# Optimization experiments

Measured on AMD Instinct MI355X. Metric: run time of the kernel, lower is better.

The kernel has to match this reference:

```python
import jax, jax.numpy as jnp
import numpy as np

NUM_HEADS = 12
NUM_LANDMARKS = 64
EPS_REG = 1e-4


def setup_inputs() -> dict:
    key = jax.random.key(0)
    k1, k2, k3 = jax.random.split(key, 3)
    B, N, C = 4, 4096, 768
    x = jax.random.normal(k1, (B, N, C), dtype=jnp.float32)
    w_qkv = jax.random.normal(k2, (3 * C, C), dtype=jnp.float32) * (C ** -0.5)
    w_proj = jax.random.normal(k3, (C, C), dtype=jnp.float32) * (C ** -0.5)
    b_proj = jnp.zeros((C,), dtype=jnp.float32)
    return {"x": x, "w_qkv": w_qkv, "w_proj": w_proj, "b_proj": b_proj}


def _landmark_pool(t, m):
    # t: [B, H, N, D]; assumes N % m == 0 (true for chosen shapes)
    B, H, N, D = t.shape
    seg = N // m
    return t.reshape(B, H, m, seg, D).mean(axis=3)


def reference(x, w_qkv, w_proj, b_proj):
    B, N, C = x.shape
    H = NUM_HEADS
    D = C // H
    m = min(NUM_LANDMARKS, N)
    scale = D ** -0.5

    qkv = x @ w_qkv.T                              # [B, N, 3C]
    qkv = qkv.reshape(B, N, 3, H, D).transpose(2, 0, 3, 1, 4)
    q, k, v = qkv[0], qkv[1], qkv[2]               # [B, H, N, D]

    q_lm = _landmark_pool(q, m)                    # [B, H, m, D]
    k_lm = _landmark_pool(k, m)                    # [B, H, m, D]

    attn_q_km = jax.nn.softmax(jnp.einsum('bhnd,bhmd->bhnm', q, k_lm) * scale, axis=-1)
    attn_qm_km = jax.nn.softmax(jnp.einsum('bhld,bhmd->bhlm', q_lm, k_lm) * scale, axis=-1)
    attn_qm_k = jax.nn.softmax(jnp.einsum('bhmd,bhnd->bhmn', q_lm, k) * scale, axis=-1)

    eye = jnp.eye(m, dtype=attn_qm_km.dtype)
    inv_mid = jnp.linalg.inv(attn_qm_km + EPS_REG * eye)   # [B, H, m, m]

    out = attn_q_km @ (inv_mid @ (attn_qm_k @ v))          # [B, H, N, D]
    out = out.transpose(0, 2, 1, 3).reshape(B, N, C)
    out = out @ w_proj.T + b_proj
    return out
```

## Files before the change

### kernel.cpp

```cpp
#include <hip/hip_runtime.h>

typedef unsigned short u16;
typedef __attribute__((ext_vector_type(8))) short bf16x8;
typedef __attribute__((ext_vector_type(8))) unsigned short u16x8;
typedef __attribute__((ext_vector_type(4))) unsigned short u16x4;
typedef __attribute__((ext_vector_type(4))) float f32x4;

#define NB 4
#define NH 12
#define NSEQ 4096
#define NC 768
#define ND 64
#define NM 64
#define NBH 48

__device__ __forceinline__ float b2f(u16 u){ unsigned v = ((unsigned)u)<<16; return __builtin_bit_cast(float, v); }
__device__ __forceinline__ u16 f2b(float f){ unsigned u = __builtin_bit_cast(unsigned, f); u = u + 0x7FFFu + ((u>>16)&1u); return (u16)(u>>16); }
__device__ __forceinline__ void split2(float f, u16& h, u16& l){
  h = f2b(f);
  l = f2b(f - b2f(h));
}

typedef const __attribute__((address_space(1))) unsigned int guint;
typedef __attribute__((address_space(3))) unsigned int luint;
__device__ __forceinline__ void gload16(const void* g, void* l){
  __builtin_amdgcn_global_load_lds((guint*)g, (luint*)l, 16, 0, 0);
}

__device__ __forceinline__ f32x4 mfma16x16(bf16x8 a, bf16x8 b, f32x4 c){
  return __builtin_amdgcn_mfma_f32_16x16x32_bf16(a, b, c, 0, 0, 0);
}

__global__ __launch_bounds__(256) void k_split(const float* __restrict__ src, u16* __restrict__ dh,
                                               u16* __restrict__ dl, int n4){
  int i = blockIdx.x*256 + threadIdx.x;
  if (i >= n4) return;
  f32x4 v = ((const f32x4*)src)[i];
  u16x4 hh, ll;
  #pragma unroll
  for (int e=0;e<4;++e){ u16 hb, lb; split2(v[e], hb, lb); hh[e]=hb; ll[e]=lb; }
  ((u16x4*)dh)[i] = hh; ((u16x4*)dl)[i] = ll;
}

__global__ __launch_bounds__(256) void k_qkv(const u16* __restrict__ xh, const u16* __restrict__ xl,
                                             const u16* __restrict__ wh, const u16* __restrict__ wl,
                                             u16* __restrict__ qh, u16* __restrict__ ql,
                                             u16* __restrict__ kh, u16* __restrict__ kl,
                                             u16* __restrict__ vh, u16* __restrict__ vl){
  __shared__ u16 Ah[8192], Al[8192], Bh[8192], Bl[8192];
  const int K = NC;
  int tid = threadIdx.x, wave = tid>>6, lane = tid&63;
  int wm = wave>>1, wn = wave&1;
  int m0 = blockIdx.y*128, n0 = blockIdx.x*128;
  int srow = lane>>3, scol = (lane&7)*8;
  const u16* src0; u16* dst0;
  if (wave==0){ src0 = xh + (size_t)m0*K; dst0 = Ah; }
  else if (wave==1){ src0 = xl + (size_t)m0*K; dst0 = Al; }
  else if (wave==2){ src0 = wh + (size_t)n0*K; dst0 = Bh; }
  else            { src0 = wl + (size_t)n0*K; dst0 = Bl; }
  f32x4 acc[4][4] = {};
  for (int k0=0; k0<K; k0+=64){
    #pragma unroll
    for (int it=0; it<16; ++it){
      int r = it*8;
      gload16(&src0[(size_t)(r+srow)*K + k0 + scol], &dst0[r*64]);
    }
    __syncthreads();
    #pragma unroll
    for (int kk=0; kk<2; ++kk){
      int koff = kk*32 + (lane>>4)*8;
      bf16x8 a_h[4], a_l[4], b_h[4], b_l[4];
      #pragma unroll
      for (int i=0;i<4;++i){
        int ro = (wm*64+i*16+(lane&15))*64 + koff;
        a_h[i] = *(const bf16x8*)&Ah[ro]; a_l[i] = *(const bf16x8*)&Al[ro];
      }
      #pragma unroll
      for (int j=0;j<4;++j){
        int ro = (wn*64+j*16+(lane&15))*64 + koff;
        b_h[j] = *(const bf16x8*)&Bh[ro]; b_l[j] = *(const bf16x8*)&Bl[ro];
      }
      #pragma unroll
      for (int i=0;i<4;++i)
        #pragma unroll
        for (int j=0;j<4;++j){
          acc[i][j] = mfma16x16(a_h[i], b_h[j], acc[i][j]);
          acc[i][j] = mfma16x16(a_h[i], b_l[j], acc[i][j]);
          acc[i][j] = mfma16x16(a_l[i], b_h[j], acc[i][j]);
        }
    }
    __syncthreads();
  }
  int rb = (lane>>4)*4, cb = lane&15;
  #pragma unroll
  for (int j=0;j<4;++j){
    int gn = n0 + wn*64 + j*16 + cb;
    int s = gn/768; int rem = gn - s*768; int hd = rem>>6, d = rem&63;
    u16* dh = (s==0)? qh : (s==1)? kh : vh;
    u16* dl = (s==0)? ql : (s==1)? kl : vl;
    #pragma unroll
    for (int i=0;i<4;++i){
      #pragma unroll
      for (int r=0;r<4;++r){
        int gm = m0 + wm*64 + i*16 + rb + r;
        int b_ = gm>>12, n = gm & 4095;
        size_t idx = (((size_t)(b_*NH + hd))*NSEQ + n)*ND + d;
        u16 hb, lb; split2(acc[i][j][r], hb, lb);
        dh[idx] = hb; dl[idx] = lb;
      }
    }
  }
}

__global__ __launch_bounds__(256) void k_proj(const u16* __restrict__ Hh, const u16* __restrict__ Hl,
                                              const u16* __restrict__ wh, const u16* __restrict__ wl,
                                              const float* __restrict__ bias, float* __restrict__ out){
  __shared__ u16 Ah[8192], Al[8192], Bh[8192], Bl[8192];
  const int K = NC;
  int tid = threadIdx.x, wave = tid>>6, lane = tid&63;
  int wm = wave>>1, wn = wave&1;
  int m0 = blockIdx.y*128, n0 = blockIdx.x*128;
  int srow = lane>>3, scol = (lane&7)*8;
  const u16* src0; u16* dst0;
  if (wave==0){ src0 = Hh + (size_t)m0*K; dst0 = Ah; }
  else if (wave==1){ src0 = Hl + (size_t)m0*K; dst0 = Al; }
  else if (wave==2){ src0 = wh + (size_t)n0*K; dst0 = Bh; }
  else            { src0 = wl + (size_t)n0*K; dst0 = Bl; }
  f32x4 acc[4][4] = {};
  for (int k0=0; k0<K; k0+=64){
    #pragma unroll
    for (int it=0; it<16; ++it){
      int r = it*8;
      gload16(&src0[(size_t)(r+srow)*K + k0 + scol], &dst0[r*64]);
    }
    __syncthreads();
    #pragma unroll
    for (int kk=0; kk<2; ++kk){
      int koff = kk*32 + (lane>>4)*8;
      bf16x8 a_h[4], a_l[4], b_h[4], b_l[4];
      #pragma unroll
      for (int i=0;i<4;++i){
        int ro = (wm*64+i*16+(lane&15))*64 + koff;
        a_h[i] = *(const bf16x8*)&Ah[ro]; a_l[i] = *(const bf16x8*)&Al[ro];
      }
      #pragma unroll
      for (int j=0;j<4;++j){
        int ro = (wn*64+j*16+(lane&15))*64 + koff;
        b_h[j] = *(const bf16x8*)&Bh[ro]; b_l[j] = *(const bf16x8*)&Bl[ro];
      }
      #pragma unroll
      for (int i=0;i<4;++i)
        #pragma unroll
        for (int j=0;j<4;++j){
          acc[i][j] = mfma16x16(a_h[i], b_h[j], acc[i][j]);
          acc[i][j] = mfma16x16(a_h[i], b_l[j], acc[i][j]);
          acc[i][j] = mfma16x16(a_l[i], b_h[j], acc[i][j]);
        }
    }
    __syncthreads();
  }
  int rb = (lane>>4)*4, cb = lane&15;
  #pragma unroll
  for (int j=0;j<4;++j){
    int gn = n0 + wn*64 + j*16 + cb;
    float bb = bias[gn];
    #pragma unroll
    for (int i=0;i<4;++i){
      #pragma unroll
      for (int r=0;r<4;++r){
        int gm = m0 + wm*64 + i*16 + rb + r;
        out[(size_t)gm*NC + gn] = acc[i][j][r] + bb;
      }
    }
  }
}

__global__ __launch_bounds__(64) void k_pool(const u16* __restrict__ qh, const u16* __restrict__ ql,
                                             const u16* __restrict__ kh, const u16* __restrict__ kl,
                                             float* __restrict__ qlmf, float* __restrict__ klmf,
                                             u16* __restrict__ qlmh, u16* __restrict__ qlml,
                                             u16* __restrict__ klmh, u16* __restrict__ klml){
  int l = blockIdx.x, bh = blockIdx.y, d = threadIdx.x;
  size_t base = ((size_t)bh*NSEQ + l*64)*ND + d;
  float sq = 0.f, sk = 0.f;
  #pragma unroll 8
  for (int j=0;j<64;++j){
    size_t o = base + (size_t)j*ND;
    sq += b2f(qh[o]) + b2f(ql[o]);
    sk += b2f(kh[o]) + b2f(kl[o]);
  }
  sq *= (1.f/64.f); sk *= (1.f/64.f);
  size_t o = ((size_t)bh*NM + l)*ND + d;
  qlmf[o] = sq; klmf[o] = sk;
  u16 hb, lb;
  split2(sq, hb, lb); qlmh[o] = hb; qlml[o] = lb;
  split2(sk, hb, lb); klmh[o] = hb; klml[o] = lb;
}

__global__ __launch_bounds__(256) void k_s2(const u16* __restrict__ qlmh, const u16* __restrict__ qlml,
                                            const u16* __restrict__ kh, const u16* __restrict__ kl,
                                            float* __restrict__ s2f){
  int chunk = blockIdx.x, bh = blockIdx.y;
  int tid = threadIdx.x, wave = tid>>6, lane = tid&63;
  const u16* Ahp = qlmh + (size_t)bh*NM*ND;
  const u16* Alp = qlml + (size_t)bh*NM*ND;
  const u16* Bhp = kh + (size_t)bh*NSEQ*ND;
  const u16* Blp = kl + (size_t)bh*NSEQ*ND;
  int nbase = chunk*256 + wave*64;
  f32x4 acc[4][4] = {};
  #pragma unroll
  for (int kk=0; kk<2; ++kk){
    int koff = kk*32 + (lane>>4)*8;
    bf16x8 a_h[4], a_l[4], b_h[4], b_l[4];
    #pragma unroll
    for (int i=0;i<4;++i){
      size_t ro = (size_t)(i*16+(lane&15))*ND + koff;
      a_h[i] = *(const bf16x8*)&Ahp[ro]; a_l[i] = *(const bf16x8*)&Alp[ro];
    }
    #pragma unroll
    for (int j=0;j<4;++j){
      size_t ro = (size_t)(nbase + j*16 + (lane&15))*ND + koff;
      b_h[j] = *(const bf16x8*)&Bhp[ro]; b_l[j] = *(const bf16x8*)&Blp[ro];
    }
    #pragma unroll
    for (int i=0;i<4;++i)
      #pragma unroll
      for (int j=0;j<4;++j){
        acc[i][j] = mfma16x16(a_h[i], b_h[j], acc[i][j]);
        acc[i][j] = mfma16x16(a_h[i], b_l[j], acc[i][j]);
        acc[i][j] = mfma16x16(a_l[i], b_h[j], acc[i][j]);
      }
  }
  int rb = (lane>>4)*4, cb = lane&15;
  #pragma unroll
  for (int i=0;i<4;++i)
    #pragma unroll
    for (int j=0;j<4;++j)
      #pragma unroll
      for (int r=0;r<4;++r){
        int l = i*16 + rb + r; int n = nbase + j*16 + cb;
        s2f[((size_t)bh*NM + l)*NSEQ + n] = acc[i][j][r]*0.125f;
      }
}

__global__ __launch_bounds__(256) void k_sm(float* __restrict__ s2region){
  int row = blockIdx.x;
  int tid = threadIdx.x, lane = tid&63, wid = tid>>6;
  __shared__ float redm[4], reds[4];
  const float* src = s2region + (size_t)row*NSEQ;
  const f32x4* ps = (const f32x4*)(src + (size_t)tid*16);
  f32x4 v0 = ps[0], v1 = ps[1], v2 = ps[2], v3 = ps[3];
  float vals[16];
  #pragma unroll
  for (int e=0;e<4;++e){ vals[e]=v0[e]; vals[4+e]=v1[e]; vals[8+e]=v2[e]; vals[12+e]=v3[e]; }
  float mx = -1e30f;
  #pragma unroll
  for (int j=0;j<16;++j) mx = fmaxf(mx, vals[j]);
  for (int off=32; off; off>>=1) mx = fmaxf(mx, __shfl_xor(mx, off));
  if (lane==0) redm[wid] = mx;
  __syncthreads();
  mx = fmaxf(fmaxf(redm[0],redm[1]), fmaxf(redm[2],redm[3]));
  float s = 0.f;
  #pragma unroll
  for (int j=0;j<16;++j){ vals[j] = __expf(vals[j]-mx); s += vals[j]; }
  for (int off=32; off; off>>=1) s += __shfl_xor(s, off);
  if (lane==0) reds[wid] = s;
  __syncthreads();
  s = reds[0]+reds[1]+reds[2]+reds[3];
  float inv = 1.f/s;
  u16* rh = (u16*)s2region + (size_t)row*8192;
  u16* rl = rh + 4096;
  u16x8 oh0, oh1, ol0, ol1;
  #pragma unroll
  for (int j=0;j<8;++j){
    u16 hb, lb;
    split2(vals[j]*inv, hb, lb);   oh0[j]=hb; ol0[j]=lb;
    split2(vals[8+j]*inv, hb, lb); oh1[j]=hb; ol1[j]=lb;
  }
  ((u16x8*)(rh + (size_t)tid*16))[0] = oh0;
  ((u16x8*)(rh + (size_t)tid*16))[1] = oh1;
  ((u16x8*)(rl + (size_t)tid*16))[0] = ol0;
  ((u16x8*)(rl + (size_t)tid*16))[1] = ol1;
}

__global__ __launch_bounds__(256) void k_transpose(const u16* __restrict__ vh, const u16* __restrict__ vl,
                                                   u16* __restrict__ vTh, u16* __restrict__ vTl){
  __shared__ u16 th[64*65], tl_[64*65];
  int bh = blockIdx.y, n0 = blockIdx.x*64, tid = threadIdx.x;
  #pragma unroll
  for (int jj=0;jj<16;++jj){
    int idx = tid + jj*256; int n = idx>>6, d = idx&63;
    size_t g = ((size_t)bh*NSEQ + n0 + n)*ND + d;
    th[n*65+d] = vh[g]; tl_[n*65+d] = vl[g];
  }
  __syncthreads();
  #pragma unroll
  for (int jj=0;jj<16;++jj){
    int idx = tid + jj*256; int d = idx>>6, n = idx&63;
    size_t g = ((size_t)bh*ND + d)*NSEQ + n0 + n;
    vTh[g] = th[n*65+d]; vTl[g] = tl_[n*65+d];
  }
}

__global__ __launch_bounds__(256) void k_t1(const u16* __restrict__ p2base, const u16* __restrict__ vTh,
                                            const u16* __restrict__ vTl, float* __restrict__ t1p){
  int kb = blockIdx.x, bh = blockIdx.y;
  int tid = threadIdx.x, wave = tid>>6, lane = tid&63;
  int arow = wave*16 + (lane&15);
  const u16* rowp = p2base + (size_t)(bh*64 + arow)*8192;
  const u16* Bh = vTh + (size_t)bh*ND*NSEQ;
  const u16* Bl = vTl + (size_t)bh*ND*NSEQ;
  f32x4 acc[4] = {};
  for (int ks=0; ks<16; ++ks){
    int koff = kb*512 + ks*32 + (lane>>4)*8;
    bf16x8 a_h = *(const bf16x8*)&rowp[koff];
    bf16x8 a_l = *(const bf16x8*)&rowp[4096 + koff];
    #pragma unroll
    for (int j=0;j<4;++j){
      size_t ro = (size_t)(j*16+(lane&15))*NSEQ + koff;
      bf16x8 b_h = *(const bf16x8*)&Bh[ro];
      bf16x8 b_l = *(const bf16x8*)&Bl[ro];
      acc[j] = mfma16x16(a_h, b_h, acc[j]);
      acc[j] = mfma16x16(a_h, b_l, acc[j]);
      acc[j] = mfma16x16(a_l, b_h, acc[j]);
    }
  }
  int rb = (lane>>4)*4, cb = lane&15;
  #pragma unroll
  for (int j=0;j<4;++j)
    #pragma unroll
    for (int r=0;r<4;++r){
      int l = wave*16 + rb + r; int d = j*16 + cb;
      t1p[((size_t)(kb*NBH + bh)*NM + l)*ND + d] = acc[j][r];
    }
}

__global__ __launch_bounds__(256) void k_mid(const float* __restrict__ qlmf, const float* __restrict__ klmf,
                                            const float* __restrict__ t1p,
                                            u16* __restrict__ w2th, u16* __restrict__ w2tl){
  __shared__ float M[64*68];
  __shared__ float T[64*68];
  __shared__ int piv_s;
  int bh = blockIdx.x, tid = threadIdx.x;
  int r = tid>>2, qd = tid&3;
  const float* qrow  = qlmf + (size_t)bh*NM*ND + r*64;
  const float* kbase = klmf + (size_t)bh*NM*ND;
  float qv[64];
  #pragma unroll
  for (int e=0;e<16;++e){
    f32x4 t4 = ((const f32x4*)qrow)[e];
    qv[e*4]=t4[0]; qv[e*4+1]=t4[1]; qv[e*4+2]=t4[2]; qv[e*4+3]=t4[3];
  }
  float sv[16];
  #pragma unroll
  for (int mi=0;mi<16;++mi){
    const float* krow = kbase + (size_t)(qd*16+mi)*64;
    float a = 0.f;
    #pragma unroll
    for (int e=0;e<16;++e){
      f32x4 k4 = ((const f32x4*)krow)[e];
      a += qv[e*4]*k4[0] + qv[e*4+1]*k4[1] + qv[e*4+2]*k4[2] + qv[e*4+3]*k4[3];
    }
    sv[mi] = a*0.125f;
  }
  float mx = sv[0];
  #pragma unroll
  for (int mi=1;mi<16;++mi) mx = fmaxf(mx, sv[mi]);
  mx = fmaxf(mx, __shfl_xor(mx,1)); mx = fmaxf(mx, __shfl_xor(mx,2));
  float sum = 0.f;
  #pragma unroll
  for (int mi=0;mi<16;++mi){ sv[mi] = __expf(sv[mi]-mx); sum += sv[mi]; }
  sum += __shfl_xor(sum,1); sum += __shfl_xor(sum,2);
  float sinv = 1.f/sum;
  #pragma unroll
  for (int mi=0;mi<16;++mi){
    int m = qd*16+mi;
    float p = sv[mi]*sinv;
    if (m == r) p += 1e-4f;
    M[r*68+m] = p;
  }
  #pragma unroll
  for (int q=0;q<4;++q){
    int c = qd*16 + q*4;
    f32x4 a = {};
    #pragma unroll
    for (int kb=0;kb<8;++kb)
      a += *(const f32x4*)&t1p[((size_t)(kb*NBH + bh)*NM + r)*ND + c];
    *(f32x4*)&T[r*68+c] = a;
  }
  __syncthreads();
  for (int kp=0; kp<64; ++kp){
    if (tid < 64){
      float val = (tid >= kp) ? fabsf(M[tid*68+kp]) : -1.f;
      int idx = tid;
      #pragma unroll
      for (int off=32; off; off>>=1){
        float ov = __shfl_xor(val, off); int oi = __shfl_xor(idx, off);
        if (ov > val || (ov == val && oi < idx)){ val = ov; idx = oi; }
      }
      if (tid == 0) piv_s = idx;
    }
    __syncthreads();
    int p = piv_s;
    if (r == kp){
      float pinv = 1.f / M[p*68+kp];
      f32x4 mk[4], mp[4], tk[4], tp_[4];
      #pragma unroll
      for (int q=0;q<4;++q){
        int c = qd*16 + q*4;
        mk[q] = *(const f32x4*)&M[kp*68+c]; mp[q] = *(const f32x4*)&M[p*68+c];
        tk[q] = *(const f32x4*)&T[kp*68+c]; tp_[q] = *(const f32x4*)&T[p*68+c];
      }
      #pragma unroll
      for (int q=0;q<4;++q){
        int c = qd*16 + q*4;
        *(f32x4*)&M[p*68+c] = mk[q];       *(f32x4*)&T[p*68+c] = tk[q];
        *(f32x4*)&M[kp*68+c] = mp[q]*pinv; *(f32x4*)&T[kp*68+c] = tp_[q]*pinv;
      }
    }
    __syncthreads();
    if (r != kp){
      float f = M[r*68+kp];
      #pragma unroll
      for (int q=0;q<4;++q){
        int c = qd*16 + q*4;
        f32x4 pm = *(const f32x4*)&M[kp*68+c];
        f32x4 om = *(const f32x4*)&M[r*68+c];
        *(f32x4*)&M[r*68+c] = om - f*pm;
        f32x4 pt = *(const f32x4*)&T[kp*68+c];
        f32x4 ot = *(const f32x4*)&T[r*68+c];
        *(f32x4*)&T[r*68+c] = ot - f*pt;
      }
    }
    __syncthreads();
  }
  int d = tid>>2, qs = tid&3;
  #pragma unroll
  for (int li=0; li<16; ++li){
    int l = qs*16 + li;
    float xv = T[l*68 + d];
    u16 hb, lb; split2(xv, hb, lb);
    size_t o = ((size_t)bh*ND + d)*NM + l;
    w2th[o] = hb; w2tl[o] = lb;
  }
}

__global__ __launch_bounds__(256) void k_final(const u16* __restrict__ qh, const u16* __restrict__ ql,
                                               const u16* __restrict__ klmh, const u16* __restrict__ klml,
                                               const u16* __restrict__ w2th, const u16* __restrict__ w2tl,
                                               u16* __restrict__ Hh, u16* __restrict__ Hl){
  __shared__ u16 Ph[4*4096], Pl[4*4096];
  int chunk = blockIdx.x, bh = blockIdx.y;
  int b_ = bh/NH, hd = bh - b_*NH;
  int tid = threadIdx.x, wave = tid>>6, lane = tid&63;
  int n0 = chunk*256 + wave*64;
  const u16* qhp = qh + ((size_t)bh*NSEQ + n0)*ND;
  const u16* qlp = ql + ((size_t)bh*NSEQ + n0)*ND;
  const u16* Kh = klmh + (size_t)bh*NM*ND;
  const u16* Kl = klml + (size_t)bh*NM*ND;
  const u16* Wh = w2th + (size_t)bh*ND*NM;
  const u16* Wl = w2tl + (size_t)bh*ND*NM;
  u16* Phw = Ph + wave*4096;
  u16* Plw = Pl + wave*4096;
  f32x4 accs[4][4] = {};
  #pragma unroll
  for (int kk=0; kk<2; ++kk){
    int koff = kk*32 + (lane>>4)*8;
    bf16x8 a_h[4], a_l[4], b_h[4], b_l[4];
    #pragma unroll
    for (int i=0;i<4;++i){
      size_t ro = (size_t)(i*16+(lane&15))*ND + koff;
      a_h[i] = *(const bf16x8*)&qhp[ro]; a_l[i] = *(const bf16x8*)&qlp[ro];
    }
    #pragma unroll
    for (int j=0;j<4;++j){
      size_t ro = (size_t)(j*16+(lane&15))*ND + koff;
      b_h[j] = *(const bf16x8*)&Kh[ro]; b_l[j] = *(const bf16x8*)&Kl[ro];
    }
    #pragma unroll
    for (int i=0;i<4;++i)
      #pragma unroll
      for (int j=0;j<4;++j){
        accs[i][j] = mfma16x16(a_h[i], b_h[j], accs[i][j]);
        accs[i][j] = mfma16x16(a_h[i], b_l[j], accs[i][j]);
        accs[i][j] = mfma16x16(a_l[i], b_h[j], accs[i][j]);
      }
  }
  #pragma unroll
  for (int i=0;i<4;++i)
    #pragma unroll
    for (int j=0;j<4;++j) accs[i][j] *= 0.125f;
  int rb = (lane>>4)*4, cb = lane&15;
  #pragma unroll
  for (int i=0;i<4;++i){
    #pragma unroll
    for (int r=0;r<4;++r){
      float mx = -1e30f;
      #pragma unroll
      for (int j=0;j<4;++j) mx = fmaxf(mx, accs[i][j][r]);
      #pragma unroll
      for (int off=1; off<16; off<<=1) mx = fmaxf(mx, __shfl_xor(mx, off));
      float e[4]; float sum = 0.f;
      #pragma unroll
      for (int j=0;j<4;++j){ e[j] = __expf(accs[i][j][r]-mx); sum += e[j]; }
      #pragma unroll
      for (int off=1; off<16; off<<=1) sum += __shfl_xor(sum, off);
      float inv = 1.f/sum;
      int row = i*16 + rb + r;
      #pragma unroll
      for (int j=0;j<4;++j){
        u16 hb, lb; split2(e[j]*inv, hb, lb);
        Phw[row*64 + j*16 + cb] = hb;
        Plw[row*64 + j*16 + cb] = lb;
      }
    }
  }
  __syncthreads();
  f32x4 acco[4][4] = {};
  #pragma unroll
  for (int kk=0; kk<2; ++kk){
    int koff = kk*32 + (lane>>4)*8;
    bf16x8 a_h[4], a_l[4], b_h[4], b_l[4];
    #pragma unroll
    for (int i=0;i<4;++i){
      int ro = (i*16+(lane&15))*64 + koff;
      a_h[i] = *(const bf16x8*)&Phw[ro]; a_l[i] = *(const bf16x8*)&Plw[ro];
    }
    #pragma unroll
    for (int j=0;j<4;++j){
      size_t ro = (size_t)(j*16+(lane&15))*64 + koff;
      b_h[j] = *(const bf16x8*)&Wh[ro]; b_l[j] = *(const bf16x8*)&Wl[ro];
    }
    #pragma unroll
    for (int i=0;i<4;++i)
      #pragma unroll
      for (int j=0;j<4;++j){
        acco[i][j] = mfma16x16(a_h[i], b_h[j], acco[i][j]);
        acco[i][j] = mfma16x16(a_h[i], b_l[j], acco[i][j]);
        acco[i][j] = mfma16x16(a_l[i], b_h[j], acco[i][j]);
      }
  }
  #pragma unroll
  for (int i=0;i<4;++i)
    #pragma unroll
    for (int j=0;j<4;++j)
      #pragma unroll
      for (int r=0;r<4;++r){
        int n = n0 + i*16 + rb + r;
        int d = j*16 + cb;
        size_t o = ((size_t)(b_*NSEQ + n))*NC + hd*64 + d;
        u16 hb, lb; split2(acco[i][j][r], hb, lb);
        Hh[o] = hb; Hl[o] = lb;
      }
}

__global__ void k_sent(float* out){ out[0] = 1.0e9f; }

#define OFF_QH     0ull
#define OFF_QL     25165824ull
#define OFF_KH     50331648ull
#define OFF_KL     75497472ull
#define OFF_VH     100663296ull
#define OFF_VL     125829120ull
#define OFF_S2     150994944ull
#define OFF_QLMF   201326592ull
#define OFF_KLMF   202113024ull
#define OFF_QLMH   202899456ull
#define OFF_QLML   203292672ull
#define OFF_KLMH   203685888ull
#define OFF_KLML   204079104ull
#define OFF_W2TH   204472320ull
#define OFF_W2TL   204865536ull
#define OFF_T1P    205258752ull
#define OFF_WQH    211550208ull
#define OFF_WQL    215089152ull
#define OFF_WPH    218628096ull
#define OFF_WPL    219807744ull
#define WS_NEEDED  220987392ull

extern "C" void kernel_launch(void* const* d_in, const int* in_sizes, int n_in,
                              void* d_out, int out_size, void* d_ws, size_t ws_size,
                              hipStream_t stream){
  const float* x     = (const float*)d_in[0];
  const float* wqkv  = (const float*)d_in[1];
  const float* wproj = (const float*)d_in[2];
  const float* bproj = (const float*)d_in[3];
  float* out = (float*)d_out;
  char* ws = (char*)d_ws;
  if (ws_size < WS_NEEDED){ k_sent<<<1,1,0,stream>>>(out); return; }
  u16* qh = (u16*)(ws + OFF_QH);  u16* ql = (u16*)(ws + OFF_QL);
  u16* kh = (u16*)(ws + OFF_KH);  u16* kl = (u16*)(ws + OFF_KL);
  u16* vh = (u16*)(ws + OFF_VH);  u16* vl = (u16*)(ws + OFF_VL);
  u16* vTh = kh; u16* vTl = kl;
  u16* xh = (u16*)(ws + OFF_S2);
  u16* xl = (u16*)(ws + OFF_S2 + 25165824ull);
  float* s2f = (float*)(ws + OFF_S2);
  u16* p2base = (u16*)(ws + OFF_S2);
  u16* Hh = (u16*)(ws + OFF_S2);
  u16* Hl = (u16*)(ws + OFF_S2 + 25165824ull);
  float* qlmf = (float*)(ws + OFF_QLMF);
  float* klmf = (float*)(ws + OFF_KLMF);
  u16* qlmh = (u16*)(ws + OFF_QLMH); u16* qlml = (u16*)(ws + OFF_QLML);
  u16* klmh = (u16*)(ws + OFF_KLMH); u16* klml = (u16*)(ws + OFF_KLML);
  u16* w2th = (u16*)(ws + OFF_W2TH); u16* w2tl = (u16*)(ws + OFF_W2TL);
  float* t1p = (float*)(ws + OFF_T1P);
  u16* wqh = (u16*)(ws + OFF_WQH); u16* wql = (u16*)(ws + OFF_WQL);
  u16* wph = (u16*)(ws + OFF_WPH); u16* wpl = (u16*)(ws + OFF_WPL);

  k_split    <<<12288, 256, 0, stream>>>(x, xh, xl, 3145728);
  k_split    <<<1728,  256, 0, stream>>>(wqkv, wqh, wql, 442368);
  k_split    <<<576,   256, 0, stream>>>(wproj, wph, wpl, 147456);
  k_qkv      <<<dim3(18,128), 256, 0, stream>>>(xh, xl, wqh, wql, qh, ql, kh, kl, vh, vl);
  k_pool     <<<dim3(64,48),   64, 0, stream>>>(qh, ql, kh, kl, qlmf, klmf, qlmh, qlml, klmh, klml);
  k_s2       <<<dim3(16,48),  256, 0, stream>>>(qlmh, qlml, kh, kl, s2f);
  k_sm       <<<3072,         256, 0, stream>>>(s2f);
  k_transpose<<<dim3(64,48),  256, 0, stream>>>(vh, vl, vTh, vTl);
  k_t1       <<<dim3(8,48),   256, 0, stream>>>(p2base, vTh, vTl, t1p);
  k_mid      <<<48,           256, 0, stream>>>(qlmf, klmf, t1p, w2th, w2tl);
  k_final    <<<dim3(16,48),  256, 0, stream>>>(qh, ql, klmh, klml, w2th, w2tl, Hh, Hl);
  k_proj     <<<dim3(6,128),  256, 0, stream>>>(Hh, Hl, wph, wpl, bproj, out);
}
```

Baseline: 559.0 us.

## Replace QKV and projection GEMMs with double-buffered 256x256 tile kernel

Both split-bf16 GEMMs now run through one templated 512-thread kernel with 256x256 tiles. It double-buffers LDS using async global-to-LDS loads, applies an XOR swizzle against bank conflicts, remaps blocks for L2 locality, and raises wave priority around the MFMA clusters. The QKV epilogue writes V directly in transposed layout, which removes the separate transpose kernel. The larger tiles mean fewer blocks (576 and 192), which risks poor CU utilisation on the projection GEMM. The 128 KB LDS footprint also limits occupancy.

```diff
diff --git a/kernel.cpp b/kernel.cpp
--- a/kernel.cpp
+++ b/kernel.cpp
@@ -42,134 +42,124 @@
   ((u16x4*)dh)[i] = hh; ((u16x4*)dl)[i] = ll;
 }
 
-__global__ __launch_bounds__(256) void k_qkv(const u16* __restrict__ xh, const u16* __restrict__ xl,
-                                             const u16* __restrict__ wh, const u16* __restrict__ wl,
-                                             u16* __restrict__ qh, u16* __restrict__ ql,
-                                             u16* __restrict__ kh, u16* __restrict__ kl,
-                                             u16* __restrict__ vh, u16* __restrict__ vl){
-  __shared__ u16 Ah[8192], Al[8192], Bh[8192], Bl[8192];
+template<int MODE>
+__global__ __launch_bounds__(512,2) void k_gemm256(
+    const u16* __restrict__ Agh, const u16* __restrict__ Agl,
+    const u16* __restrict__ Bgh, const u16* __restrict__ Bgl,
+    u16* __restrict__ q_h, u16* __restrict__ q_l,
+    u16* __restrict__ k_h, u16* __restrict__ k_l,
+    u16* __restrict__ v_h, u16* __restrict__ v_l,
+    const float* __restrict__ bias, float* __restrict__ outf,
+    int nbx){
+  __shared__ u16 lds[65536];
   const int K = NC;
   int tid = threadIdx.x, wave = tid>>6, lane = tid&63;
-  int wm = wave>>1, wn = wave&1;
-  int m0 = blockIdx.y*128, n0 = blockIdx.x*128;
-  int srow = lane>>3, scol = (lane&7)*8;
-  const u16* src0; u16* dst0;
-  if (wave==0){ src0 = xh + (size_t)m0*K; dst0 = Ah; }
-  else if (wave==1){ src0 = xl + (size_t)m0*K; dst0 = Al; }
-  else if (wave==2){ src0 = wh + (size_t)n0*K; dst0 = Bh; }
-  else            { src0 = wl + (size_t)n0*K; dst0 = Bl; }
-  f32x4 acc[4][4] = {};
-  for (int k0=0; k0<K; k0+=64){
-    #pragma unroll
-    for (int it=0; it<16; ++it){
-      int r = it*8;
-      gload16(&src0[(size_t)(r+srow)*K + k0 + scol], &dst0[r*64]);
-    }
-    __syncthreads();
-    #pragma unroll
-    for (int kk=0; kk<2; ++kk){
-      int koff = kk*32 + (lane>>4)*8;
-      bf16x8 a_h[4], a_l[4], b_h[4], b_l[4];
-      #pragma unroll
-      for (int i=0;i<4;++i){
-        int ro = (wm*64+i*16+(lane&15))*64 + koff;
-        a_h[i] = *(const bf16x8*)&Ah[ro]; a_l[i] = *(const bf16x8*)&Al[ro];
-      }
+  int wm = wave>>2, wn = wave&3;
+  int nwg = gridDim.x, bid = blockIdx.x;
+  int swz = (bid&7)*(nwg>>3) + (bid>>3);
+  int by = swz / nbx, bx = swz - by*nbx;
+  int m0 = by*256, n0 = bx*256;
+  const u16* sbase[8]; int soff[8];
+  #pragma unroll
+  for (int s=0;s<8;++s){
+    int c = s*512 + tid;
+    int mat = c>>10, idx = c&1023, row = idx>>2, slot = idx&3;
+    int gslot = slot ^ ((row>>1)&3);
+    const u16* g;
+    if (mat==0)      g = Agh + (size_t)(m0+row)*K + gslot*8;
+    else if (mat==1) g = Agl + (size_t)(m0+row)*K + gslot*8;
+    else if (mat==2) g = Bgh + (size_t)(n0+row)*K + gslot*8;
+    else             g = Bgl + (size_t)(n0+row)*K + gslot*8;
+    sbase[s] = g;
+    soff[s] = mat*8192 + row*32 + slot*8;
+  }
+  int fr = ((lane&15)>>1)&3;
+  int sl = ((lane>>4) ^ fr)*8;
+  int aoff = (wm*128 + (lane&15))*32 + sl;
+  int boff = (wn*64  + (lane&15))*32 + sl;
+  #pragma unroll
+  for (int s=0;s<8;++s) gload16(sbase[s], &lds[soff[s]]);
+  asm volatile("s_waitcnt vmcnt(0)" ::: "memory");
+  __builtin_amdgcn_s_barrier();
+  __builtin_amdgcn_sched_barrier(0);
+  f32x4 acc[8][4] = {};
+  for (int t=0; t<24; ++t){
+    int cur = (t&1)*32768, nxt = ((t+1)&1)*32768;
+    int k0 = (t+1)*32;
+    bool st = (t < 23);
+    const u16* Ab = &lds[cur];
+    const u16* Bb = &lds[cur + 16384];
+    if (st){
+      gload16(sbase[0]+k0, &lds[nxt+soff[0]]); gload16(sbase[1]+k0, &lds[nxt+soff[1]]);
+      gload16(sbase[2]+k0, &lds[nxt+soff[2]]); gload16(sbase[3]+k0, &lds[nxt+soff[3]]);
+    }
+    bf16x8 bh[4], bl[4];
+    #pragma unroll
+    for (int j=0;j<4;++j){
+      bh[j] = *(const bf16x8*)&Bb[boff + j*512];
+      bl[j] = *(const bf16x8*)&Bb[8192 + boff + j*512];
+    }
+    #pragma unroll
+    for (int p=0;p<4;++p){
+      if (st && p==1){
+        gload16(sbase[4]+k0, &lds[nxt+soff[4]]); gload16(sbase[5]+k0, &lds[nxt+soff[5]]);
+        gload16(sbase[6]+k0, &lds[nxt+soff[6]]); gload16(sbase[7]+k0, &lds[nxt+soff[7]]);
+      }
+      bf16x8 ah0 = *(const bf16x8*)&Ab[aoff + (2*p)*512];
+      bf16x8 al0 = *(const bf16x8*)&Ab[8192 + aoff + (2*p)*512];
+      bf16x8 ah1 = *(const bf16x8*)&Ab[aoff + (2*p+1)*512];
+      bf16x8 al1 = *(const bf16x8*)&Ab[8192 + aoff + (2*p+1)*512];
+      __builtin_amdgcn_s_setprio(1);
       #pragma unroll
       for (int j=0;j<4;++j){
-        int ro = (wn*64+j*16+(lane&15))*64 + koff;
-        b_h[j] = *(const bf16x8*)&Bh[ro]; b_l[j] = *(const bf16x8*)&Bl[ro];
-      }
-      #pragma unroll
-      for (int i=0;i<4;++i)
+        acc[2*p][j]   = mfma16x16(ah0, bh[j], acc[2*p][j]);
+        acc[2*p][j]   = mfma16x16(ah0, bl[j], acc[2*p][j]);
+        acc[2*p][j]   = mfma16x16(al0, bh[j], acc[2*p][j]);
+        acc[2*p+1][j] = mfma16x16(ah1, bh[j], acc[2*p+1][j]);
+        acc[2*p+1][j] = mfma16x16(ah1, bl[j], acc[2*p+1][j]);
+        acc[2*p+1][j] = mfma16x16(al1, bh[j], acc[2*p+1][j]);
+      }
+      __builtin_amdgcn_s_setprio(0);
+      if (p < 3) __builtin_amdgcn_s_barrier();
+    }
+    asm volatile("s_waitcnt vmcnt(0)" ::: "memory");
+    __builtin_amdgcn_s_barrier();
+    __builtin_amdgcn_sched_barrier(0);
+  }
+  int rb = (lane>>4)*4, cb = lane&15;
+  if (MODE == 0){
+    #pragma unroll
+    for (int j=0;j<4;++j){
+      int gn = n0 + wn*64 + j*16 + cb;
+      int s = gn/768; int rem = gn - s*768; int hd = rem>>6, d = rem&63;
+      u16* dh = (s==0)? q_h : (s==1)? k_h : v_h;
+      u16* dl = (s==0)? q_l : (s==1)? k_l : v_l;
+      #pragma unroll
+      for (int i=0;i<8;++i){
         #pragma unroll
-        for (int j=0;j<4;++j){
-          acc[i][j] = mfma16x16(a_h[i], b_h[j], acc[i][j]);
-          acc[i][j] = mfma16x16(a_h[i], b_l[j], acc[i][j]);
-          acc[i][j] = mfma16x16(a_l[i], b_h[j], acc[i][j]);
+        for (int r=0;r<4;++r){
+          int gm = m0 + wm*128 + i*16 + rb + r;
+          int b_ = gm>>12, n = gm & 4095;
+          size_t idx;
+          if (s==2) idx = (((size_t)(b_*NH + hd))*ND + d)*NSEQ + n;
+          else      idx = (((size_t)(b_*NH + hd))*NSEQ + n)*ND + d;
+          u16 hb2, lb2; split2(acc[i][j][r], hb2, lb2);
+          dh[idx] = hb2; dl[idx] = lb2;
         }
-    }
-    __syncthreads();
-  }
-  int rb = (lane>>4)*4, cb = lane&15;
-  #pragma unroll
-  for (int j=0;j<4;++j){
-    int gn = n0 + wn*64 + j*16 + cb;
-    int s = gn/768; int rem = gn - s*768; int hd = rem>>6, d = rem&63;
-    u16* dh = (s==0)? qh : (s==1)? kh : vh;
-    u16* dl = (s==0)? ql : (s==1)? kl : vl;
-    #pragma unroll
-    for (int i=0;i<4;++i){
-      #pragma unroll
-      for (int r=0;r<4;++r){
-        int gm = m0 + wm*64 + i*16 + rb + r;
-        int b_ = gm>>12, n = gm & 4095;
-        size_t idx = (((size_t)(b_*NH + hd))*NSEQ + n)*ND + d;
-        u16 hb, lb; split2(acc[i][j][r], hb, lb);
-        dh[idx] = hb; dl[idx] = lb;
-      }
-    }
-  }
-}
-
-__global__ __launch_bounds__(256) void k_proj(const u16* __restrict__ Hh, const u16* __restrict__ Hl,
-                                              const u16* __restrict__ wh, const u16* __restrict__ wl,
-                                              const float* __restrict__ bias, float* __restrict__ out){
-  __shared__ u16 Ah[8192], Al[8192], Bh[8192], Bl[8192];
-  const int K = NC;
-  int tid = threadIdx.x, wave = tid>>6, lane = tid&63;
-  int wm = wave>>1, wn = wave&1;
-  int m0 = blockIdx.y*128, n0 = blockIdx.x*128;
-  int srow = lane>>3, scol = (lane&7)*8;
-  const u16* src0; u16* dst0;
-  if (wave==0){ src0 = Hh + (size_t)m0*K; dst0 = Ah; }
-  else if (wave==1){ src0 = Hl + (size_t)m0*K; dst0 = Al; }
-  else if (wave==2){ src0 = wh + (size_t)n0*K; dst0 = Bh; }
-  else            { src0 = wl + (size_t)n0*K; dst0 = Bl; }
-  f32x4 acc[4][4] = {};
-  for (int k0=0; k0<K; k0+=64){
-    #pragma unroll
-    for (int it=0; it<16; ++it){
-      int r = it*8;
-      gload16(&src0[(size_t)(r+srow)*K + k0 + scol], &dst0[r*64]);
-    }
-    __syncthreads();
-    #pragma unroll
-    for (int kk=0; kk<2; ++kk){
-      int koff = kk*32 + (lane>>4)*8;
-      bf16x8 a_h[4], a_l[4], b_h[4], b_l[4];
-      #pragma unroll
-      for (int i=0;i<4;++i){
-        int ro = (wm*64+i*16+(lane&15))*64 + koff;
-        a_h[i] = *(const bf16x8*)&Ah[ro]; a_l[i] = *(const bf16x8*)&Al[ro];
-      }
-      #pragma unroll
-      for (int j=0;j<4;++j){
-        int ro = (wn*64+j*16+(lane&15))*64 + koff;
-        b_h[j] = *(const bf16x8*)&Bh[ro]; b_l[j] = *(const bf16x8*)&Bl[ro];
-      }
-      #pragma unroll
-      for (int i=0;i<4;++i)
+      }
+    }
+  } else {
+    #pragma unroll
+    for (int j=0;j<4;++j){
+      int gn = n0 + wn*64 + j*16 + cb;
+      float bb = bias[gn];
+      #pragma unroll
+      for (int i=0;i<8;++i){
         #pragma unroll
-        for (int j=0;j<4;++j){
-          acc[i][j] = mfma16x16(a_h[i], b_h[j], acc[i][j]);
-          acc[i][j] = mfma16x16(a_h[i], b_l[j], acc[i][j]);
-          acc[i][j] = mfma16x16(a_l[i], b_h[j], acc[i][j]);
+        for (int r=0;r<4;++r){
+          int gm = m0 + wm*128 + i*16 + rb + r;
+          outf[(size_t)gm*NC + gn] = acc[i][j][r] + bb;
         }
-    }
-    __syncthreads();
-  }
-  int rb = (lane>>4)*4, cb = lane&15;
-  #pragma unroll
-  for (int j=0;j<4;++j){
-    int gn = n0 + wn*64 + j*16 + cb;
-    float bb = bias[gn];
-    #pragma unroll
-    for (int i=0;i<4;++i){
-      #pragma unroll
-      for (int r=0;r<4;++r){
-        int gm = m0 + wm*64 + i*16 + rb + r;
-        out[(size_t)gm*NC + gn] = acc[i][j][r] + bb;
       }
     }
   }
@@ -281,25 +271,6 @@
   ((u16x8*)(rh + (size_t)tid*16))[1] = oh1;
   ((u16x8*)(rl + (size_t)tid*16))[0] = ol0;
   ((u16x8*)(rl + (size_t)tid*16))[1] = ol1;
-}
-
-__global__ __launch_bounds__(256) void k_transpose(const u16* __restrict__ vh, const u16* __restrict__ vl,
-                                                   u16* __restrict__ vTh, u16* __restrict__ vTl){
-  __shared__ u16 th[64*65], tl_[64*65];
-  int bh = blockIdx.y, n0 = blockIdx.x*64, tid = threadIdx.x;
-  #pragma unroll
-  for (int jj=0;jj<16;++jj){
-    int idx = tid + jj*256; int n = idx>>6, d = idx&63;
-    size_t g = ((size_t)bh*NSEQ + n0 + n)*ND + d;
-    th[n*65+d] = vh[g]; tl_[n*65+d] = vl[g];
-  }
-  __syncthreads();
-  #pragma unroll
-  for (int jj=0;jj<16;++jj){
-    int idx = tid + jj*256; int d = idx>>6, n = idx&63;
-    size_t g = ((size_t)bh*ND + d)*NSEQ + n0 + n;
-    vTh[g] = th[n*65+d]; vTl[g] = tl_[n*65+d];
-  }
 }
 
 __global__ __launch_bounds__(256) void k_t1(const u16* __restrict__ p2base, const u16* __restrict__ vTh,
@@ -560,8 +531,8 @@
 #define OFF_QL     25165824ull
 #define OFF_KH     50331648ull
 #define OFF_KL     75497472ull
-#define OFF_VH     100663296ull
-#define OFF_VL     125829120ull
+#define OFF_VTH    100663296ull
+#define OFF_VTL    125829120ull
 #define OFF_S2     150994944ull
 #define OFF_QLMF   201326592ull
 #define OFF_KLMF   202113024ull
@@ -590,8 +561,7 @@
   if (ws_size < WS_NEEDED){ k_sent<<<1,1,0,stream>>>(out); return; }
   u16* qh = (u16*)(ws + OFF_QH);  u16* ql = (u16*)(ws + OFF_QL);
   u16* kh = (u16*)(ws + OFF_KH);  u16* kl = (u16*)(ws + OFF_KL);
-  u16* vh = (u16*)(ws + OFF_VH);  u16* vl = (u16*)(ws + OFF_VL);
-  u16* vTh = kh; u16* vTl = kl;
+  u16* vTh = (u16*)(ws + OFF_VTH); u16* vTl = (u16*)(ws + OFF_VTL);
   u16* xh = (u16*)(ws + OFF_S2);
   u16* xl = (u16*)(ws + OFF_S2 + 25165824ull);
   float* s2f = (float*)(ws + OFF_S2);
@@ -607,16 +577,18 @@
   u16* wqh = (u16*)(ws + OFF_WQH); u16* wql = (u16*)(ws + OFF_WQL);
   u16* wph = (u16*)(ws + OFF_WPH); u16* wpl = (u16*)(ws + OFF_WPL);
 
-  k_split    <<<12288, 256, 0, stream>>>(x, xh, xl, 3145728);
-  k_split    <<<1728,  256, 0, stream>>>(wqkv, wqh, wql, 442368);
-  k_split    <<<576,   256, 0, stream>>>(wproj, wph, wpl, 147456);
-  k_qkv      <<<dim3(18,128), 256, 0, stream>>>(xh, xl, wqh, wql, qh, ql, kh, kl, vh, vl);
-  k_pool     <<<dim3(64,48),   64, 0, stream>>>(qh, ql, kh, kl, qlmf, klmf, qlmh, qlml, klmh, klml);
-  k_s2       <<<dim3(16,48),  256, 0, stream>>>(qlmh, qlml, kh, kl, s2f);
-  k_sm       <<<3072,         256, 0, stream>>>(s2f);
-  k_transpose<<<dim3(64,48),  256, 0, stream>>>(vh, vl, vTh, vTl);
-  k_t1       <<<dim3(8,48),   256, 0, stream>>>(p2base, vTh, vTl, t1p);
-  k_mid      <<<48,           256, 0, stream>>>(qlmf, klmf, t1p, w2th, w2tl);
-  k_final    <<<dim3(16,48),  256, 0, stream>>>(qh, ql, klmh, klml, w2th, w2tl, Hh, Hl);
-  k_proj     <<<dim3(6,128),  256, 0, stream>>>(Hh, Hl, wph, wpl, bproj, out);
-}
+  k_split      <<<12288, 256, 0, stream>>>(x, xh, xl, 3145728);
+  k_split      <<<1728,  256, 0, stream>>>(wqkv, wqh, wql, 442368);
+  k_split      <<<576,   256, 0, stream>>>(wproj, wph, wpl, 147456);
+  k_gemm256<0> <<<576, 512, 0, stream>>>(xh, xl, wqh, wql, qh, ql, kh, kl, vTh, vTl,
+                                         nullptr, nullptr, 9);
+  k_pool       <<<dim3(64,48),  64, 0, stream>>>(qh, ql, kh, kl, qlmf, klmf, qlmh, qlml, klmh, klml);
+  k_s2         <<<dim3(16,48), 256, 0, stream>>>(qlmh, qlml, kh, kl, s2f);
+  k_sm         <<<3072,        256, 0, stream>>>(s2f);
+  k_t1         <<<dim3(8,48),  256, 0, stream>>>(p2base, vTh, vTl, t1p);
+  k_mid        <<<48,          256, 0, stream>>>(qlmf, klmf, t1p, w2th, w2tl);
+  k_final      <<<dim3(16,48), 256, 0, stream>>>(qh, ql, klmh, klml, w2th, w2tl, Hh, Hl);
+  k_gemm256<1> <<<192, 512, 0, stream>>>(Hh, Hl, wph, wpl,
+                                         nullptr, nullptr, nullptr, nullptr, nullptr, nullptr,
+                                         bproj, out, 3);
+}
```

After: 582.6 us. 1.04x slower.

## Write V transposed from QKV GEMM and XOR-swizzle LDS tiles

Applied to the files above, without the earlier changes.

The QKV GEMM epilogue now writes V straight into a [B,H,D,N] transposed layout, so the separate transpose kernel and its extra read/write pass over V are gone. The LDS tiles in the QKV, projection and final kernels get an XOR swizzle on the 8-element column chunk, applied on the global-to-LDS load and on the fragment reads, to reduce LDS bank conflicts. In exchange, the V stores in the GEMM epilogue become strided along N, which may coalesce less well than the old row-major writes.

```diff
diff --git a/kernel.cpp b/kernel.cpp
--- a/kernel.cpp
+++ b/kernel.cpp
@@ -42,17 +42,19 @@
   ((u16x4*)dh)[i] = hh; ((u16x4*)dl)[i] = ll;
 }
 
+
 __global__ __launch_bounds__(256) void k_qkv(const u16* __restrict__ xh, const u16* __restrict__ xl,
                                              const u16* __restrict__ wh, const u16* __restrict__ wl,
                                              u16* __restrict__ qh, u16* __restrict__ ql,
                                              u16* __restrict__ kh, u16* __restrict__ kl,
-                                             u16* __restrict__ vh, u16* __restrict__ vl){
+                                             u16* __restrict__ vTh, u16* __restrict__ vTl){
   __shared__ u16 Ah[8192], Al[8192], Bh[8192], Bl[8192];
   const int K = NC;
   int tid = threadIdx.x, wave = tid>>6, lane = tid&63;
   int wm = wave>>1, wn = wave&1;
   int m0 = blockIdx.y*128, n0 = blockIdx.x*128;
-  int srow = lane>>3, scol = (lane&7)*8;
+  int srow = lane>>3;
+  int scol = ((lane&7) ^ srow)*8;
   const u16* src0; u16* dst0;
   if (wave==0){ src0 = xh + (size_t)m0*K; dst0 = Ah; }
   else if (wave==1){ src0 = xl + (size_t)m0*K; dst0 = Al; }
@@ -68,16 +70,16 @@
     __syncthreads();
     #pragma unroll
     for (int kk=0; kk<2; ++kk){
-      int koff = kk*32 + (lane>>4)*8;
+      int sl = ((kk*4 + (lane>>4)) ^ (lane&7))*8;
       bf16x8 a_h[4], a_l[4], b_h[4], b_l[4];
       #pragma unroll
       for (int i=0;i<4;++i){
-        int ro = (wm*64+i*16+(lane&15))*64 + koff;
+        int ro = (wm*64+i*16+(lane&15))*64 + sl;
         a_h[i] = *(const bf16x8*)&Ah[ro]; a_l[i] = *(const bf16x8*)&Al[ro];
       }
       #pragma unroll
       for (int j=0;j<4;++j){
-        int ro = (wn*64+j*16+(lane&15))*64 + koff;
+        int ro = (wn*64+j*16+(lane&15))*64 + sl;
         b_h[j] = *(const bf16x8*)&Bh[ro]; b_l[j] = *(const bf16x8*)&Bl[ro];
       }
       #pragma unroll
@@ -96,15 +98,17 @@
   for (int j=0;j<4;++j){
     int gn = n0 + wn*64 + j*16 + cb;
     int s = gn/768; int rem = gn - s*768; int hd = rem>>6, d = rem&63;
-    u16* dh = (s==0)? qh : (s==1)? kh : vh;
-    u16* dl = (s==0)? ql : (s==1)? kl : vl;
+    u16* dh = (s==0)? qh : (s==1)? kh : vTh;
+    u16* dl = (s==0)? ql : (s==1)? kl : vTl;
     #pragma unroll
     for (int i=0;i<4;++i){
       #pragma unroll
       for (int r=0;r<4;++r){
         int gm = m0 + wm*64 + i*16 + rb + r;
         int b_ = gm>>12, n = gm & 4095;
-        size_t idx = (((size_t)(b_*NH + hd))*NSEQ + n)*ND + d;
+        size_t idx;
+        if (s==2) idx = (((size_t)(b_*NH + hd))*ND + d)*NSEQ + n;
+        else      idx = (((size_t)(b_*NH + hd))*NSEQ + n)*ND + d;
         u16 hb, lb; split2(acc[i][j][r], hb, lb);
         dh[idx] = hb; dl[idx] = lb;
       }
@@ -120,7 +124,8 @@
   int tid = threadIdx.x, wave = tid>>6, lane = tid&63;
   int wm = wave>>1, wn = wave&1;
   int m0 = blockIdx.y*128, n0 = blockIdx.x*128;
-  int srow = lane>>3, scol = (lane&7)*8;
+  int srow = lane>>3;
+  int scol = ((lane&7) ^ srow)*8;
   const u16* src0; u16* dst0;
   if (wave==0){ src0 = Hh + (size_t)m0*K; dst0 = Ah; }
   else if (wave==1){ src0 = Hl + (size_t)m0*K; dst0 = Al; }
@@ -136,16 +141,16 @@
     __syncthreads();
     #pragma unroll
     for (int kk=0; kk<2; ++kk){
-      int koff = kk*32 + (lane>>4)*8;
+      int sl = ((kk*4 + (lane>>4)) ^ (lane&7))*8;
       bf16x8 a_h[4], a_l[4], b_h[4], b_l[4];
       #pragma unroll
       for (int i=0;i<4;++i){
-        int ro = (wm*64+i*16+(lane&15))*64 + koff;
+        int ro = (wm*64+i*16+(lane&15))*64 + sl;
         a_h[i] = *(const bf16x8*)&Ah[ro]; a_l[i] = *(const bf16x8*)&Al[ro];
       }
       #pragma unroll
       for (int j=0;j<4;++j){
-        int ro = (wn*64+j*16+(lane&15))*64 + koff;
+        int ro = (wn*64+j*16+(lane&15))*64 + sl;
         b_h[j] = *(const bf16x8*)&Bh[ro]; b_l[j] = *(const bf16x8*)&Bl[ro];
       }
       #pragma unroll
@@ -281,25 +286,6 @@
   ((u16x8*)(rh + (size_t)tid*16))[1] = oh1;
   ((u16x8*)(rl + (size_t)tid*16))[0] = ol0;
   ((u16x8*)(rl + (size_t)tid*16))[1] = ol1;
-}
-
-__global__ __launch_bounds__(256) void k_transpose(const u16* __restrict__ vh, const u16* __restrict__ vl,
-                                                   u16* __restrict__ vTh, u16* __restrict__ vTl){
-  __shared__ u16 th[64*65], tl_[64*65];
-  int bh = blockIdx.y, n0 = blockIdx.x*64, tid = threadIdx.x;
-  #pragma unroll
-  for (int jj=0;jj<16;++jj){
-    int idx = tid + jj*256; int n = idx>>6, d = idx&63;
-    size_t g = ((size_t)bh*NSEQ + n0 + n)*ND + d;
-    th[n*65+d] = vh[g]; tl_[n*65+d] = vl[g];
-  }
-  __syncthreads();
-  #pragma unroll
-  for (int jj=0;jj<16;++jj){
-    int idx = tid + jj*256; int d = idx>>6, n = idx&63;
-    size_t g = ((size_t)bh*ND + d)*NSEQ + n0 + n;
-    vTh[g] = th[n*65+d]; vTl[g] = tl_[n*65+d];
-  }
 }
 
 __global__ __launch_bounds__(256) void k_t1(const u16* __restrict__ p2base, const u16* __restrict__ vTh,
@@ -510,8 +496,10 @@
       #pragma unroll
       for (int j=0;j<4;++j){
         u16 hb, lb; split2(e[j]*inv, hb, lb);
-        Phw[row*64 + j*16 + cb] = hb;
-        Plw[row*64 + j*16 + cb] = lb;
+        int col = j*16 + cb;
+        int scol = (((col>>3) ^ (row&7))<<3) | (col&7);
+        Phw[row*64 + scol] = hb;
+        Plw[row*64 + scol] = lb;
       }
     }
   }
@@ -520,10 +508,11 @@
   #pragma unroll
   for (int kk=0; kk<2; ++kk){
     int koff = kk*32 + (lane>>4)*8;
+    int sl = ((kk*4 + (lane>>4)) ^ (lane&7))*8;
     bf16x8 a_h[4], a_l[4], b_h[4], b_l[4];
     #pragma unroll
     for (int i=0;i<4;++i){
-      int ro = (i*16+(lane&15))*64 + koff;
+      int ro = (i*16+(lane&15))*64 + sl;
       a_h[i] = *(const bf16x8*)&Phw[ro]; a_l[i] = *(const bf16x8*)&Plw[ro];
     }
     #pragma unroll
@@ -560,8 +549,8 @@
 #define OFF_QL     25165824ull
 #define OFF_KH     50331648ull
 #define OFF_KL     75497472ull
-#define OFF_VH     100663296ull
-#define OFF_VL     125829120ull
+#define OFF_VTH    100663296ull
+#define OFF_VTL    125829120ull
 #define OFF_S2     150994944ull
 #define OFF_QLMF   201326592ull
 #define OFF_KLMF   202113024ull
@@ -590,8 +579,7 @@
   if (ws_size < WS_NEEDED){ k_sent<<<1,1,0,stream>>>(out); return; }
   u16* qh = (u16*)(ws + OFF_QH);  u16* ql = (u16*)(ws + OFF_QL);
   u16* kh = (u16*)(ws + OFF_KH);  u16* kl = (u16*)(ws + OFF_KL);
-  u16* vh = (u16*)(ws + OFF_VH);  u16* vl = (u16*)(ws + OFF_VL);
-  u16* vTh = kh; u16* vTl = kl;
+  u16* vTh = (u16*)(ws + OFF_VTH); u16* vTl = (u16*)(ws + OFF_VTL);
   u16* xh = (u16*)(ws + OFF_S2);
   u16* xl = (u16*)(ws + OFF_S2 + 25165824ull);
   float* s2f = (float*)(ws + OFF_S2);
@@ -610,11 +598,10 @@
   k_split    <<<12288, 256, 0, stream>>>(x, xh, xl, 3145728);
   k_split    <<<1728,  256, 0, stream>>>(wqkv, wqh, wql, 442368);
   k_split    <<<576,   256, 0, stream>>>(wproj, wph, wpl, 147456);
-  k_qkv      <<<dim3(18,128), 256, 0, stream>>>(xh, xl, wqh, wql, qh, ql, kh, kl, vh, vl);
+  k_qkv      <<<dim3(18,128), 256, 0, stream>>>(xh, xl, wqh, wql, qh, ql, kh, kl, vTh, vTl);
   k_pool     <<<dim3(64,48),   64, 0, stream>>>(qh, ql, kh, kl, qlmf, klmf, qlmh, qlml, klmh, klml);
   k_s2       <<<dim3(16,48),  256, 0, stream>>>(qlmh, qlml, kh, kl, s2f);
   k_sm       <<<3072,         256, 0, stream>>>(s2f);
-  k_transpose<<<dim3(64,48),  256, 0, stream>>>(vh, vl, vTh, vTl);
   k_t1       <<<dim3(8,48),   256, 0, stream>>>(p2base, vTh, vTl, t1p);
   k_mid      <<<48,           256, 0, stream>>>(qlmf, klmf, t1p, w2th, w2tl);
   k_final    <<<dim3(16,48),  256, 0, stream>>>(qh, ql, klmh, klml, w2th, w2tl, Hh, Hl);
```

Result: slower. 580.4 us (+3.8%).
